# Kernel tuning notes

Hardware: AMD Instinct MI355X
Metric: run time of the kernel (lower is better)

Reference implementation:

```python
import jax, jax.numpy as jnp
import numpy as np


def conv1d(x, w, b):
    # x: [B, Cin, L], w: [Cout, Cin, K] (torch layout), padding=1
    out = jax.lax.conv_general_dilated(
        x, w, window_strides=(1,), padding=[(1, 1)],
        dimension_numbers=('NCH', 'OIH', 'NCH'))
    return out + b[None, :, None]


def maxpool2(x):
    # MaxPool1d(kernel=2, stride=2) on last dim
    return jax.lax.reduce_window(x, -jnp.inf, jax.lax.max,
                                 (1, 1, 2), (1, 1, 2), 'VALID')


def build_edges(B, n):
    # bidirectional chain edges per graph + self-loops (GCNConv default)
    base = (jnp.arange(B) * n)[:, None]          # [B,1]
    i = jnp.arange(n - 1)[None, :]               # [1,n-1]
    s = (base + i).reshape(-1)
    d = s + 1
    loop = jnp.arange(B * n)
    src = jnp.concatenate([s, d, loop])
    dst = jnp.concatenate([d, s, loop])
    return src, dst


def gcn_conv(x, w, b, src, dst, deg_isqrt, n_total):
    # PyG GCNConv: X' = D^-1/2 (A+I) D^-1/2 (X W) + b
    h = x @ w                                    # [N, Dout]
    norm = deg_isqrt[src] * deg_isqrt[dst]       # [E]
    agg = jax.ops.segment_sum(h[src] * norm[:, None], dst,
                              num_segments=n_total)
    return agg + b


def setup_inputs() -> dict:
    key = jax.random.key(0)
    ks = jax.random.split(key, 12)
    B, L = 64, 16384
    CF, H, NC = 8, 64, 2
    sd = lambda fan_in: 1.0 / np.sqrt(fan_in)
    return {
        'x': jax.random.normal(ks[0], (B, 1, L), jnp.float32),
        'batch_size': B,
        'conv1_w': jax.random.normal(ks[1], (CF, 1, 3), jnp.float32) * sd(3),
        'conv1_b': jax.random.normal(ks[2], (CF,), jnp.float32) * 0.01,
        'conv2_w': jax.random.normal(ks[3], (CF, CF, 3), jnp.float32) * sd(3 * CF),
        'conv2_b': jax.random.normal(ks[4], (CF,), jnp.float32) * 0.01,
        'gcn1_w': jax.random.normal(ks[5], (CF, H), jnp.float32) * sd(CF),
        'gcn1_b': jax.random.normal(ks[6], (H,), jnp.float32) * 0.01,
        'gcn2_w': jax.random.normal(ks[7], (H, H), jnp.float32) * sd(H),
        'gcn2_b': jax.random.normal(ks[8], (H,), jnp.float32) * 0.01,
        'fc_w': jax.random.normal(ks[9], (H, NC), jnp.float32) * sd(H),
        'fc_b': jax.random.normal(ks[10], (NC,), jnp.float32) * 0.01,
    }


def reference(x, batch_size, conv1_w, conv1_b, conv2_w, conv2_b,
              gcn1_w, gcn1_b, gcn2_w, gcn2_b, fc_w, fc_b):
    # CNN feature extractor
    h = maxpool2(jax.nn.relu(conv1d(x, conv1_w, conv1_b)))
    h = maxpool2(jax.nn.relu(conv1d(h, conv2_w, conv2_b)))
    h = jnp.transpose(h, (0, 2, 1))              # [B, n, CF]
    B, n, C = h.shape
    N = B * n
    nodes = h.reshape(N, C)
    # line-graph message passing (GCNConv x2), dropout is identity at eval
    src, dst = build_edges(B, n)
    deg = jax.ops.segment_sum(jnp.ones_like(dst, jnp.float32), dst,
                              num_segments=N)
    deg_isqrt = jax.lax.rsqrt(deg)
    h1 = jax.nn.relu(gcn_conv(nodes, gcn1_w, gcn1_b, src, dst, deg_isqrt, N))
    h2 = jax.nn.relu(gcn_conv(h1, gcn2_w, gcn2_b, src, dst, deg_isqrt, N))
    # global_mean_pool: nodes are contiguous per graph
    pooled = h2.reshape(B, n, -1).mean(axis=1)   # [B, H]
    return pooled @ fc_w + fc_b                  # [B, num_classes]
```

## Files before the change

### kernel.cpp

```cpp
#include <hip/hip_runtime.h>
#include <hip/hip_bf16.h>

typedef __attribute__((ext_vector_type(8))) short short8_t;
typedef __attribute__((ext_vector_type(4))) float f32x4;

#define BATCH 64
#define L0 16384
#define L1 8192
#define NPG 4096
#define CF 8
#define H 64
#define CHUNK 128
#define NCHUNK 32
#define NCHUNKS_TOTAL (BATCH * NCHUNK)

#define A_H1    0
#define A_X     0
#define A_T1    2144
#define A_ND    6528
#define A_SA    20736
#define A_RED   23040
#define ARENA_BYTES 24064

__device__ __forceinline__ float disv(int p) {
    if (p < 0 || p >= NPG) return 0.f;
    if (p == 0 || p == NPG - 1) return 0.70710678118654752f;
    return 0.57735026918962576f;
}

__device__ __forceinline__ unsigned pack_bf2(float a, float b) {
    union { __hip_bfloat162 h2; unsigned u; } cv;
    cv.h2 = __float22bfloat162_rn(make_float2(a, b));
    return cv.u;
}

__device__ __forceinline__ unsigned short bfu(float f) {
    union { __hip_bfloat16 h; unsigned short u; } cv;
    cv.h = __float2bfloat16(f);
    return cv.u;
}

__device__ __forceinline__ float lof(unsigned u) { return __uint_as_float(u << 16); }
__device__ __forceinline__ float hif(unsigned u) { return __uint_as_float(u & 0xffff0000u); }

__global__ __launch_bounds__(256) void k_prep(
        const float* __restrict__ g1w, const float* __restrict__ g2w,
        const float* __restrict__ c2w,
        unsigned short* __restrict__ w1f, unsigned short* __restrict__ w2f,
        unsigned short* __restrict__ wcf) {
    int tid = threadIdx.x;
    const float T = 1.f / 3.f;
    for (int e = tid; e < 4096; e += 256) {
        int i = e & 7, lane = (e >> 3) & 63, ks = (e >> 9) & 1, ct = e >> 10;
        int k = ks * 32 + (lane >> 4) * 8 + i;
        int n = ct * 16 + (lane & 15);
        w2f[e] = bfu(g2w[k * H + n] * T);
    }
    for (int e = tid; e < 2048; e += 256) {
        int i = e & 7, lane = (e >> 3) & 63, ct = e >> 9;
        int k = (lane >> 4) * 8 + i;
        int n = ct * 16 + (lane & 15);
        w1f[e] = (k < CF) ? bfu(g1w[k * H + n] * T) : (unsigned short)0;
    }
    for (int e = tid; e < 512; e += 256) {
        int i = e & 7, lane = e >> 3;
        int qq = lane >> 4, n = lane & 15;
        wcf[e] = (n < CF && qq < 3) ? bfu(c2w[(n * CF + i) * 3 + qq])
                                    : (unsigned short)0;
    }
}

__global__ __launch_bounds__(256, 5) void k_fused(const float* __restrict__ x,
        const float* __restrict__ c1w, const float* __restrict__ c1b,
        const float* __restrict__ c2b,
        const unsigned short* __restrict__ w1f,
        const unsigned short* __restrict__ w2f,
        const unsigned short* __restrict__ wcf,
        const float* __restrict__ g1b, const float* __restrict__ g2b,
        float* __restrict__ partials) {
    __shared__ __align__(16) char arena[ARENA_BYTES];
    float*          x_l  = (float*)(arena + A_X);
    unsigned short* t1_l = (unsigned short*)(arena + A_T1);
    float*          nd_l = (float*)(arena + A_ND);
    unsigned short* sa_l = (unsigned short*)(arena + A_SA);
    unsigned short* h1_l = (unsigned short*)(arena + A_H1);
    float*          red  = (float*)(arena + A_RED);

    const int tid = threadIdx.x;
    const int wave = tid >> 6;
    const int l = tid & 63;
    const int m = l & 15, q = l >> 4;

    const int chunk = blockIdx.x;
    const int b = chunk >> 5, ch = chunk & 31;
    const int s = ch * CHUNK;
    const bool edgeblk = (ch == 0) || (ch == NCHUNK - 1);

    const f32x4 z4 = {0.f, 0.f, 0.f, 0.f};

    {
        const float* xb = x + (size_t)b * L0;
        for (int c = tid; c < 536; c += 256) {
            int col = 4 * s - 11 + c;
            x_l[c] = (col >= 0 && col < L0) ? xb[col] : 0.f;
        }
    }
    __syncthreads();

    {
        int c0 = (tid & 3) * 2;
        float wA0 = c1w[c0 * 3], wB0 = c1w[c0 * 3 + 1], wC0 = c1w[c0 * 3 + 2];
        float wA1 = c1w[c0 * 3 + 3], wB1 = c1w[c0 * 3 + 4], wC1 = c1w[c0 * 3 + 5];
        float bb0 = c1b[c0], bb1 = c1b[c0 + 1];
        for (int v = tid; v < 274 * 4; v += 256) {
            int t = v >> 2;
            int g = 2 * s - 5 + t;
            unsigned o = 0;
            if (t < 266 && g >= 0 && g < L1) {
                float a0 = x_l[2 * t], a1 = x_l[2 * t + 1];
                float a2 = x_l[2 * t + 2], a3 = x_l[2 * t + 3];
                float y00 = bb0 + wA0 * a0 + wB0 * a1 + wC0 * a2;
                float y01 = bb0 + wA0 * a1 + wB0 * a2 + wC0 * a3;
                float y10 = bb1 + wA1 * a0 + wB1 * a1 + wC1 * a2;
                float y11 = bb1 + wA1 * a1 + wB1 * a2 + wC1 * a3;
                o = pack_bf2(fmaxf(fmaxf(y00, y01), 0.f),
                             fmaxf(fmaxf(y10, y11), 0.f));
            }
            *(unsigned*)&t1_l[t * 8 + c0] = o;
        }
    }
    __syncthreads();

    {
        short8_t wcfr = ((const short8_t*)wcf)[l];
        float bb2 = (m < CF) ? c2b[m] : 0.f;
        for (int rt = wave; rt < 17; rt += 4) {
            short8_t a = {0, 0, 0, 0, 0, 0, 0, 0};
            if (q < 3) a = *(const short8_t*)&t1_l[(rt * 16 + m + q) * 8];
            f32x4 c = __builtin_amdgcn_mfma_f32_16x16x32_bf16(a, wcfr, z4, 0, 0, 0);
            if (m < CF) {
                int n0 = rt * 8 + q * 2;
                if (n0 < 132)
                    nd_l[n0 * 8 + m] = fmaxf(fmaxf(c[0], c[1]) + bb2, 0.f);
                if (n0 + 1 < 132)
                    nd_l[(n0 + 1) * 8 + m] = fmaxf(fmaxf(c[2], c[3]) + bb2, 0.f);
            }
        }
    }
    __syncthreads();

    for (int v = tid; v < 288; v += 256) {
        int r = v >> 1, half = v & 1;
        uint2 o = {0u, 0u};
        if (r < 130) {
            float4 lo = *(const float4*)&nd_l[r * 8 + half * 4];
            float4 mi = *(const float4*)&nd_l[(r + 1) * 8 + half * 4];
            float4 hi = *(const float4*)&nd_l[(r + 2) * 8 + half * 4];
            float o0, o1, o2, o3;
            if (!edgeblk) {
                o0 = lo.x + mi.x + hi.x; o1 = lo.y + mi.y + hi.y;
                o2 = lo.z + mi.z + hi.z; o3 = lo.w + mi.w + hi.w;
            } else {
                int p = s - 1 + r;
                float dc = disv(p);
                float cm_ = 3.f * dc * dc;
                float cl_ = 3.f * dc * disv(p - 1);
                float cr_ = 3.f * dc * disv(p + 1);
                o0 = cm_ * mi.x + cl_ * lo.x + cr_ * hi.x;
                o1 = cm_ * mi.y + cl_ * lo.y + cr_ * hi.y;
                o2 = cm_ * mi.z + cl_ * lo.z + cr_ * hi.z;
                o3 = cm_ * mi.w + cl_ * lo.w + cr_ * hi.w;
            }
            o.x = pack_bf2(o0, o1);
            o.y = pack_bf2(o2, o3);
        }
        *(uint2*)&sa_l[r * 8 + half * 4] = o;
    }
    __syncthreads();

    {
        short8_t w1fr[4];
        float b1v[4];
        #pragma unroll
        for (int ct = 0; ct < 4; ++ct) {
            w1fr[ct] = ((const short8_t*)w1f)[ct * 64 + l];
            b1v[ct] = g1b[ct * 16 + m];
        }
        for (int rt = wave; rt < 9; rt += 4) {
            short8_t a = *(const short8_t*)&sa_l[(rt * 16 + m) * 8];
            int base = rt * 16 + q * 4;
            #pragma unroll
            for (int ct = 0; ct < 4; ++ct) {
                f32x4 c = __builtin_amdgcn_mfma_f32_16x16x32_bf16(a, w1fr[ct], z4, 0, 0, 0);
                float r0v = fmaxf(c[0] + b1v[ct], 0.f);
                float r1v = fmaxf(c[1] + b1v[ct], 0.f);
                float r2v = fmaxf(c[2] + b1v[ct], 0.f);
                float r3v = fmaxf(c[3] + b1v[ct], 0.f);
                unsigned p01 = pack_bf2(r0v, r1v);
                unsigned p23 = pack_bf2(r2v, r3v);
                int col = ct * 16 + m;
                h1_l[(base + 0) * 72 + col] = (unsigned short)p01;
                h1_l[(base + 1) * 72 + col] = (unsigned short)(p01 >> 16);
                h1_l[(base + 2) * 72 + col] = (unsigned short)p23;
                h1_l[(base + 3) * 72 + col] = (unsigned short)(p23 >> 16);
            }
        }
    }
    __syncthreads();

    {
        short8_t w2fr[4][2];
        float b2v[4];
        #pragma unroll
        for (int ct = 0; ct < 4; ++ct) {
            w2fr[ct][0] = ((const short8_t*)w2f)[(ct * 2 + 0) * 64 + l];
            w2fr[ct][1] = ((const short8_t*)w2f)[(ct * 2 + 1) * 64 + l];
            b2v[ct] = g2b[ct * 16 + m];
        }
        float pool_acc[4] = {0.f, 0.f, 0.f, 0.f};
        for (int rt = wave; rt < 8; rt += 4) {
            f32x4 accg[4] = {z4, z4, z4, z4};
            int r0 = rt * 16 + m;
            float cl_ = 0.f, cm_ = 0.f, cr_ = 0.f;
            if (edgeblk) {
                int p = s + r0;
                float dcp = disv(p);
                cm_ = 3.f * dcp * dcp;
                cl_ = 3.f * dcp * disv(p - 1);
                cr_ = 3.f * dcp * disv(p + 1);
            }
            #pragma unroll
            for (int ks = 0; ks < 2; ++ks) {
                int koff = ks * 32 + q * 8;
                uint4 lo = *(const uint4*)&h1_l[r0 * 72 + koff];
                uint4 mi = *(const uint4*)&h1_l[(r0 + 1) * 72 + koff];
                uint4 hi = *(const uint4*)&h1_l[(r0 + 2) * 72 + koff];
                union { unsigned u[4]; short8_t s8; } a2;
                #define A2COMP(e, UL, UM, UH)                                     \
                  { float sl, sh;                                                 \
                    if (!edgeblk) {                                               \
                        sl = lof(UL) + lof(UM) + lof(UH);                         \
                        sh = hif(UL) + hif(UM) + hif(UH);                         \
                    } else {                                                      \
                        sl = cm_ * lof(UM) + cl_ * lof(UL) + cr_ * lof(UH);       \
                        sh = cm_ * hif(UM) + cl_ * hif(UL) + cr_ * hif(UH);       \
                    }                                                             \
                    a2.u[e] = pack_bf2(sl, sh); }
                A2COMP(0, lo.x, mi.x, hi.x)
                A2COMP(1, lo.y, mi.y, hi.y)
                A2COMP(2, lo.z, mi.z, hi.z)
                A2COMP(3, lo.w, mi.w, hi.w)
                #undef A2COMP
                #pragma unroll
                for (int ct = 0; ct < 4; ++ct)
                    accg[ct] = __builtin_amdgcn_mfma_f32_16x16x32_bf16(
                        a2.s8, w2fr[ct][ks], accg[ct], 0, 0, 0);
            }
            #pragma unroll
            for (int ct = 0; ct < 4; ++ct)
                #pragma unroll
                for (int i = 0; i < 4; ++i)
                    pool_acc[ct] += fmaxf(accg[ct][i] + b2v[ct], 0.f);
        }

        #pragma unroll
        for (int ct = 0; ct < 4; ++ct) {
            float v = pool_acc[ct];
            v += __shfl_xor(v, 16);
            v += __shfl_xor(v, 32);
            if (q == 0) red[wave * 64 + ct * 16 + m] = v;
        }
    }
    __syncthreads();
    if (tid < H) {
        partials[(size_t)chunk * H + tid] = red[tid] + red[64 + tid]
                                          + red[128 + tid] + red[192 + tid];
    }
}

__global__ __launch_bounds__(256) void k_final(const float* __restrict__ partials,
        const float* __restrict__ fcw, const float* __restrict__ fcb,
        float* __restrict__ out) {
    __shared__ float red[4][H];
    __shared__ float pool_l[H];
    int bgr = blockIdx.x;
    int tid = threadIdx.x;
    int g = tid >> 6, j = tid & 63;
    float acc = 0.f;
    for (int c = g; c < NCHUNK; c += 4)
        acc += partials[((size_t)bgr * NCHUNK + c) * H + j];
    red[g][j] = acc;
    __syncthreads();
    if (tid < H)
        pool_l[j] = (red[0][j] + red[1][j] + red[2][j] + red[3][j]) * (1.f / NPG);
    __syncthreads();
    if (tid < 2) {
        float o = fcb[tid];
        for (int k = 0; k < H; ++k) o += pool_l[k] * fcw[k * 2 + tid];
        out[bgr * 2 + tid] = o;
    }
}

extern "C" void kernel_launch(void* const* d_in, const int* in_sizes, int n_in,
                              void* d_out, int out_size, void* d_ws, size_t ws_size,
                              hipStream_t stream) {
    (void)in_sizes; (void)n_in; (void)out_size; (void)ws_size;
    const float* x   = (const float*)d_in[0];
    const float* c1w = (const float*)d_in[2];
    const float* c1b = (const float*)d_in[3];
    const float* c2w = (const float*)d_in[4];
    const float* c2b = (const float*)d_in[5];
    const float* g1w = (const float*)d_in[6];
    const float* g1b = (const float*)d_in[7];
    const float* g2w = (const float*)d_in[8];
    const float* g2b = (const float*)d_in[9];
    const float* fcw = (const float*)d_in[10];
    const float* fcb = (const float*)d_in[11];
    float* out = (float*)d_out;

    float* partials = (float*)d_ws;
    unsigned short* w2f = (unsigned short*)(partials + (size_t)NCHUNKS_TOTAL * H);
    unsigned short* w1f = w2f + 4096;
    unsigned short* wcf = w1f + 2048;

    k_prep<<<1, 256, 0, stream>>>(g1w, g2w, c2w, w1f, w2f, wcf);
    k_fused<<<NCHUNKS_TOTAL, 256, 0, stream>>>(x, c1w, c1b, c2b,
                                               w1f, w2f, wcf, g1b, g2b, partials);
    k_final<<<BATCH, 256, 0, stream>>>(partials, fcw, fcb, out);
}
```

Before: 30.27 us.

## Fuse weight prep and final reduction into main kernel with atomic outputs

```diff
diff --git a/kernel.cpp b/kernel.cpp
--- a/kernel.cpp
+++ b/kernel.cpp
@@ -14,13 +14,16 @@
 #define NCHUNK 32
 #define NCHUNKS_TOTAL (BATCH * NCHUNK)
 
+#define A_W1T   0
+#define A_WCT   4096
+#define A_X     5120
+#define A_T1    7264
+#define A_ND    11520
 #define A_H1    0
-#define A_X     0
-#define A_T1    2144
-#define A_ND    6528
-#define A_SA    20736
-#define A_RED   23040
-#define ARENA_BYTES 24064
+#define A_W2T   18720
+#define A_SA    26912
+#define A_RED   28992
+#define ARENA_BYTES 30016
 
 __device__ __forceinline__ float disv(int p) {
     if (p < 0 || p >= NPG) return 0.f;
@@ -33,71 +36,63 @@
     cv.h2 = __float22bfloat162_rn(make_float2(a, b));
     return cv.u;
 }
-
 __device__ __forceinline__ unsigned short bfu(float f) {
     union { __hip_bfloat16 h; unsigned short u; } cv;
     cv.h = __float2bfloat16(f);
     return cv.u;
 }
-
 __device__ __forceinline__ float lof(unsigned u) { return __uint_as_float(u << 16); }
 __device__ __forceinline__ float hif(unsigned u) { return __uint_as_float(u & 0xffff0000u); }
 
-__global__ __launch_bounds__(256) void k_prep(
-        const float* __restrict__ g1w, const float* __restrict__ g2w,
-        const float* __restrict__ c2w,
-        unsigned short* __restrict__ w1f, unsigned short* __restrict__ w2f,
-        unsigned short* __restrict__ wcf) {
-    int tid = threadIdx.x;
+__global__ __launch_bounds__(256, 5) void k_fused(const float* __restrict__ x,
+        const float* __restrict__ c1w, const float* __restrict__ c1b,
+        const float* __restrict__ c2w, const float* __restrict__ c2b,
+        const float* __restrict__ g1w, const float* __restrict__ g1b,
+        const float* __restrict__ g2w, const float* __restrict__ g2b,
+        const float* __restrict__ fcw, const float* __restrict__ fcb,
+        float* __restrict__ out) {
+    __shared__ __align__(16) char arena[ARENA_BYTES];
+    unsigned short* w1t  = (unsigned short*)(arena + A_W1T);
+    unsigned short* wct  = (unsigned short*)(arena + A_WCT);
+    float*          x_l  = (float*)(arena + A_X);
+    unsigned short* t1_l = (unsigned short*)(arena + A_T1);
+    unsigned short* nd_l = (unsigned short*)(arena + A_ND);
+    unsigned short* h1_l = (unsigned short*)(arena + A_H1);
+    unsigned short* w2t  = (unsigned short*)(arena + A_W2T);
+    unsigned short* sa_l = (unsigned short*)(arena + A_SA);
+    float*          red  = (float*)(arena + A_RED);
+
+    const int tid = threadIdx.x;
+    const int wave = tid >> 6;
+    const int l = tid & 63;
+    const int m = l & 15, q = l >> 4;
+
+    const int chunk = blockIdx.x;
+    const int b = chunk >> 5, ch = chunk & 31;
+    const int s = ch * CHUNK;
+    const bool edgeblk = (ch == 0) || (ch == NCHUNK - 1);
+
+    const f32x4 z4 = {0.f, 0.f, 0.f, 0.f};
     const float T = 1.f / 3.f;
+
     for (int e = tid; e < 4096; e += 256) {
         int i = e & 7, lane = (e >> 3) & 63, ks = (e >> 9) & 1, ct = e >> 10;
         int k = ks * 32 + (lane >> 4) * 8 + i;
         int n = ct * 16 + (lane & 15);
-        w2f[e] = bfu(g2w[k * H + n] * T);
+        w2t[e] = bfu(g2w[k * H + n] * T);
     }
     for (int e = tid; e < 2048; e += 256) {
         int i = e & 7, lane = (e >> 3) & 63, ct = e >> 9;
         int k = (lane >> 4) * 8 + i;
         int n = ct * 16 + (lane & 15);
-        w1f[e] = (k < CF) ? bfu(g1w[k * H + n] * T) : (unsigned short)0;
+        w1t[e] = (k < CF) ? bfu(g1w[k * H + n] * T) : (unsigned short)0;
     }
     for (int e = tid; e < 512; e += 256) {
         int i = e & 7, lane = e >> 3;
         int qq = lane >> 4, n = lane & 15;
-        wcf[e] = (n < CF && qq < 3) ? bfu(c2w[(n * CF + i) * 3 + qq])
+        wct[e] = (n < CF && qq < 3) ? bfu(c2w[(n * CF + i) * 3 + qq])
                                     : (unsigned short)0;
     }
-}
-
-__global__ __launch_bounds__(256, 5) void k_fused(const float* __restrict__ x,
-        const float* __restrict__ c1w, const float* __restrict__ c1b,
-        const float* __restrict__ c2b,
-        const unsigned short* __restrict__ w1f,
-        const unsigned short* __restrict__ w2f,
-        const unsigned short* __restrict__ wcf,
-        const float* __restrict__ g1b, const float* __restrict__ g2b,
-        float* __restrict__ partials) {
-    __shared__ __align__(16) char arena[ARENA_BYTES];
-    float*          x_l  = (float*)(arena + A_X);
-    unsigned short* t1_l = (unsigned short*)(arena + A_T1);
-    float*          nd_l = (float*)(arena + A_ND);
-    unsigned short* sa_l = (unsigned short*)(arena + A_SA);
-    unsigned short* h1_l = (unsigned short*)(arena + A_H1);
-    float*          red  = (float*)(arena + A_RED);
-
-    const int tid = threadIdx.x;
-    const int wave = tid >> 6;
-    const int l = tid & 63;
-    const int m = l & 15, q = l >> 4;
-
-    const int chunk = blockIdx.x;
-    const int b = chunk >> 5, ch = chunk & 31;
-    const int s = ch * CHUNK;
-    const bool edgeblk = (ch == 0) || (ch == NCHUNK - 1);
-
-    const f32x4 z4 = {0.f, 0.f, 0.f, 0.f};
-
     {
         const float* xb = x + (size_t)b * L0;
         for (int c = tid; c < 536; c += 256) {
@@ -107,16 +102,17 @@
     }
     __syncthreads();
 
+    short8_t wcfr = ((const short8_t*)wct)[l];
     {
         int c0 = (tid & 3) * 2;
         float wA0 = c1w[c0 * 3], wB0 = c1w[c0 * 3 + 1], wC0 = c1w[c0 * 3 + 2];
         float wA1 = c1w[c0 * 3 + 3], wB1 = c1w[c0 * 3 + 4], wC1 = c1w[c0 * 3 + 5];
         float bb0 = c1b[c0], bb1 = c1b[c0 + 1];
-        for (int v = tid; v < 274 * 4; v += 256) {
+        for (int v = tid; v < 266 * 4; v += 256) {
             int t = v >> 2;
             int g = 2 * s - 5 + t;
             unsigned o = 0;
-            if (t < 266 && g >= 0 && g < L1) {
+            if (g >= 0 && g < L1) {
                 float a0 = x_l[2 * t], a1 = x_l[2 * t + 1];
                 float a2 = x_l[2 * t + 2], a3 = x_l[2 * t + 3];
                 float y00 = bb0 + wA0 * a0 + wB0 * a1 + wC0 * a2;
@@ -132,77 +128,71 @@
     __syncthreads();
 
     {
-        short8_t wcfr = ((const short8_t*)wcf)[l];
         float bb2 = (m < CF) ? c2b[m] : 0.f;
         for (int rt = wave; rt < 17; rt += 4) {
-            short8_t a = {0, 0, 0, 0, 0, 0, 0, 0};
-            if (q < 3) a = *(const short8_t*)&t1_l[(rt * 16 + m + q) * 8];
+            int rr = rt * 16 + m + q;
+            rr = rr > 265 ? 265 : rr;
+            short8_t a = *(const short8_t*)&t1_l[rr * 8];
             f32x4 c = __builtin_amdgcn_mfma_f32_16x16x32_bf16(a, wcfr, z4, 0, 0, 0);
             if (m < CF) {
                 int n0 = rt * 8 + q * 2;
                 if (n0 < 132)
-                    nd_l[n0 * 8 + m] = fmaxf(fmaxf(c[0], c[1]) + bb2, 0.f);
+                    nd_l[n0 * 8 + m] = bfu(fmaxf(fmaxf(c[0], c[1]) + bb2, 0.f));
                 if (n0 + 1 < 132)
-                    nd_l[(n0 + 1) * 8 + m] = fmaxf(fmaxf(c[2], c[3]) + bb2, 0.f);
-            }
-        }
-    }
-    __syncthreads();
-
-    for (int v = tid; v < 288; v += 256) {
+                    nd_l[(n0 + 1) * 8 + m] = bfu(fmaxf(fmaxf(c[2], c[3]) + bb2, 0.f));
+            }
+        }
+    }
+    __syncthreads();
+
+    short8_t w1fr[4];
+    float4 b1v[4];
+    #pragma unroll
+    for (int ct = 0; ct < 4; ++ct) {
+        w1fr[ct] = ((const short8_t*)w1t)[ct * 64 + l];
+        b1v[ct] = *(const float4*)&g1b[ct * 16 + q * 4];
+    }
+    for (int v = tid; v < 260; v += 256) {
         int r = v >> 1, half = v & 1;
-        uint2 o = {0u, 0u};
-        if (r < 130) {
-            float4 lo = *(const float4*)&nd_l[r * 8 + half * 4];
-            float4 mi = *(const float4*)&nd_l[(r + 1) * 8 + half * 4];
-            float4 hi = *(const float4*)&nd_l[(r + 2) * 8 + half * 4];
-            float o0, o1, o2, o3;
-            if (!edgeblk) {
-                o0 = lo.x + mi.x + hi.x; o1 = lo.y + mi.y + hi.y;
-                o2 = lo.z + mi.z + hi.z; o3 = lo.w + mi.w + hi.w;
-            } else {
-                int p = s - 1 + r;
-                float dc = disv(p);
-                float cm_ = 3.f * dc * dc;
-                float cl_ = 3.f * dc * disv(p - 1);
-                float cr_ = 3.f * dc * disv(p + 1);
-                o0 = cm_ * mi.x + cl_ * lo.x + cr_ * hi.x;
-                o1 = cm_ * mi.y + cl_ * lo.y + cr_ * hi.y;
-                o2 = cm_ * mi.z + cl_ * lo.z + cr_ * hi.z;
-                o3 = cm_ * mi.w + cl_ * lo.w + cr_ * hi.w;
-            }
-            o.x = pack_bf2(o0, o1);
-            o.y = pack_bf2(o2, o3);
-        }
-        *(uint2*)&sa_l[r * 8 + half * 4] = o;
-    }
-    __syncthreads();
-
-    {
-        short8_t w1fr[4];
-        float b1v[4];
+        uint2 RL = *(const uint2*)&nd_l[r * 8 + half * 4];
+        uint2 RM = *(const uint2*)&nd_l[(r + 1) * 8 + half * 4];
+        uint2 RH = *(const uint2*)&nd_l[(r + 2) * 8 + half * 4];
+        float o0, o1, o2, o3;
+        if (!edgeblk) {
+            o0 = lof(RL.x) + lof(RM.x) + lof(RH.x);
+            o1 = hif(RL.x) + hif(RM.x) + hif(RH.x);
+            o2 = lof(RL.y) + lof(RM.y) + lof(RH.y);
+            o3 = hif(RL.y) + hif(RM.y) + hif(RH.y);
+        } else {
+            int p = s - 1 + r;
+            float dc = disv(p);
+            float cm_ = 3.f * dc * dc;
+            float cl_ = 3.f * dc * disv(p - 1);
+            float cr_ = 3.f * dc * disv(p + 1);
+            o0 = cm_ * lof(RM.x) + cl_ * lof(RL.x) + cr_ * lof(RH.x);
+            o1 = cm_ * hif(RM.x) + cl_ * hif(RL.x) + cr_ * hif(RH.x);
+            o2 = cm_ * lof(RM.y) + cl_ * lof(RL.y) + cr_ * lof(RH.y);
+            o3 = cm_ * hif(RM.y) + cl_ * hif(RL.y) + cr_ * hif(RH.y);
+        }
+        *(uint2*)&sa_l[r * 8 + half * 4] = make_uint2(pack_bf2(o0, o1),
+                                                      pack_bf2(o2, o3));
+    }
+    __syncthreads();
+
+    for (int rt = wave; rt < 9; rt += 4) {
+        int rc = rt * 16 + m;
+        int rcc = rc > 129 ? 129 : rc;
+        short8_t sfr = *(const short8_t*)&sa_l[rcc * 8];
+        bool wok = rc < 130;
         #pragma unroll
         for (int ct = 0; ct < 4; ++ct) {
-            w1fr[ct] = ((const short8_t*)w1f)[ct * 64 + l];
-            b1v[ct] = g1b[ct * 16 + m];
-        }
-        for (int rt = wave; rt < 9; rt += 4) {
-            short8_t a = *(const short8_t*)&sa_l[(rt * 16 + m) * 8];
-            int base = rt * 16 + q * 4;
-            #pragma unroll
-            for (int ct = 0; ct < 4; ++ct) {
-                f32x4 c = __builtin_amdgcn_mfma_f32_16x16x32_bf16(a, w1fr[ct], z4, 0, 0, 0);
-                float r0v = fmaxf(c[0] + b1v[ct], 0.f);
-                float r1v = fmaxf(c[1] + b1v[ct], 0.f);
-                float r2v = fmaxf(c[2] + b1v[ct], 0.f);
-                float r3v = fmaxf(c[3] + b1v[ct], 0.f);
-                unsigned p01 = pack_bf2(r0v, r1v);
-                unsigned p23 = pack_bf2(r2v, r3v);
-                int col = ct * 16 + m;
-                h1_l[(base + 0) * 72 + col] = (unsigned short)p01;
-                h1_l[(base + 1) * 72 + col] = (unsigned short)(p01 >> 16);
-                h1_l[(base + 2) * 72 + col] = (unsigned short)p23;
-                h1_l[(base + 3) * 72 + col] = (unsigned short)(p23 >> 16);
+            f32x4 c = __builtin_amdgcn_mfma_f32_16x16x32_bf16(w1fr[ct], sfr, z4, 0, 0, 0);
+            if (wok) {
+                unsigned p01 = pack_bf2(fmaxf(c[0] + b1v[ct].x, 0.f),
+                                        fmaxf(c[1] + b1v[ct].y, 0.f));
+                unsigned p23 = pack_bf2(fmaxf(c[2] + b1v[ct].z, 0.f),
+                                        fmaxf(c[3] + b1v[ct].w, 0.f));
+                *(uint2*)&h1_l[rc * 72 + ct * 16 + q * 4] = make_uint2(p01, p23);
             }
         }
     }
@@ -213,8 +203,8 @@
         float b2v[4];
         #pragma unroll
         for (int ct = 0; ct < 4; ++ct) {
-            w2fr[ct][0] = ((const short8_t*)w2f)[(ct * 2 + 0) * 64 + l];
-            w2fr[ct][1] = ((const short8_t*)w2f)[(ct * 2 + 1) * 64 + l];
+            w2fr[ct][0] = ((const short8_t*)w2t)[(ct * 2 + 0) * 64 + l];
+            w2fr[ct][1] = ((const short8_t*)w2t)[(ct * 2 + 1) * 64 + l];
             b2v[ct] = g2b[ct * 16 + m];
         }
         float pool_acc[4] = {0.f, 0.f, 0.f, 0.f};
@@ -262,7 +252,6 @@
                 for (int i = 0; i < 4; ++i)
                     pool_acc[ct] += fmaxf(accg[ct][i] + b2v[ct], 0.f);
         }
-
         #pragma unroll
         for (int ct = 0; ct < 4; ++ct) {
             float v = pool_acc[ct];
@@ -272,39 +261,31 @@
         }
     }
     __syncthreads();
+
     if (tid < H) {
-        partials[(size_t)chunk * H + tid] = red[tid] + red[64 + tid]
-                                          + red[128 + tid] + red[192 + tid];
-    }
-}
-
-__global__ __launch_bounds__(256) void k_final(const float* __restrict__ partials,
-        const float* __restrict__ fcw, const float* __restrict__ fcb,
-        float* __restrict__ out) {
-    __shared__ float red[4][H];
-    __shared__ float pool_l[H];
-    int bgr = blockIdx.x;
-    int tid = threadIdx.x;
-    int g = tid >> 6, j = tid & 63;
-    float acc = 0.f;
-    for (int c = g; c < NCHUNK; c += 4)
-        acc += partials[((size_t)bgr * NCHUNK + c) * H + j];
-    red[g][j] = acc;
-    __syncthreads();
-    if (tid < H)
-        pool_l[j] = (red[0][j] + red[1][j] + red[2][j] + red[3][j]) * (1.f / NPG);
-    __syncthreads();
-    if (tid < 2) {
-        float o = fcb[tid];
-        for (int k = 0; k < H; ++k) o += pool_l[k] * fcw[k * 2 + tid];
-        out[bgr * 2 + tid] = o;
+        float v = red[tid] + red[64 + tid] + red[128 + tid] + red[192 + tid];
+        float s0 = v * fcw[tid * 2 + 0];
+        float s1 = v * fcw[tid * 2 + 1];
+        #pragma unroll
+        for (int o = 32; o; o >>= 1) {
+            s0 += __shfl_down(s0, o);
+            s1 += __shfl_down(s1, o);
+        }
+        if (tid == 0) {
+            atomicAdd(&out[b * 2 + 0], s0 * (1.f / NPG));
+            atomicAdd(&out[b * 2 + 1], s1 * (1.f / NPG));
+            if (ch == 0) {
+                atomicAdd(&out[b * 2 + 0], fcb[0]);
+                atomicAdd(&out[b * 2 + 1], fcb[1]);
+            }
+        }
     }
 }
 
 extern "C" void kernel_launch(void* const* d_in, const int* in_sizes, int n_in,
                               void* d_out, int out_size, void* d_ws, size_t ws_size,
                               hipStream_t stream) {
-    (void)in_sizes; (void)n_in; (void)out_size; (void)ws_size;
+    (void)in_sizes; (void)n_in; (void)d_ws; (void)ws_size;
     const float* x   = (const float*)d_in[0];
     const float* c1w = (const float*)d_in[2];
     const float* c1b = (const float*)d_in[3];
@@ -318,13 +299,7 @@
     const float* fcb = (const float*)d_in[11];
     float* out = (float*)d_out;
 
-    float* partials = (float*)d_ws;
-    unsigned short* w2f = (unsigned short*)(partials + (size_t)NCHUNKS_TOTAL * H);
-    unsigned short* w1f = w2f + 4096;
-    unsigned short* wcf = w1f + 2048;
-
-    k_prep<<<1, 256, 0, stream>>>(g1w, g2w, c2w, w1f, w2f, wcf);
-    k_fused<<<NCHUNKS_TOTAL, 256, 0, stream>>>(x, c1w, c1b, c2b,
-                                               w1f, w2f, wcf, g1b, g2b, partials);
-    k_final<<<BATCH, 256, 0, stream>>>(partials, fcw, fcb, out);
-}
+    hipMemsetAsync(out, 0, (size_t)out_size * sizeof(float), stream);
+    k_fused<<<NCHUNKS_TOTAL, 256, 0, stream>>>(x, c1w, c1b, c2w, c2b,
+                                               g1w, g1b, g2w, g2b, fcw, fcb, out);
+}
```

After: 48.60 us. 60.6% more time.
